# Kernel tuning notes

Measured on AMD Instinct MI355X. Metric: run time of the kernel, lower is better.

Reference implementation:

```python
import jax, jax.numpy as jnp
import numpy as np

TEMPERATURE = 0.07
BASE_TEMPERATURE = 0.07


def _supcon_one(feat, labels):
    # feat: [B, V, D], labels: [B]  (contrast_mode='all')
    B, V, D = feat.shape
    N = V * B
    # torch.cat(torch.unbind(feat, dim=1), dim=0): view-major ordering
    contrast = jnp.swapaxes(feat, 0, 1).reshape(N, D)  # [N, D]
    logits = jnp.einsum('nd,md->nm', contrast, contrast) / TEMPERATURE  # [N, N]
    # subtract detached row max for numerical stability
    logits = logits - jax.lax.stop_gradient(jnp.max(logits, axis=1, keepdims=True))
    pos = (labels[:, None] == labels[None, :]).astype(feat.dtype)  # [B, B]
    mask = jnp.tile(pos, (V, V))                                   # [N, N]
    logits_mask = 1.0 - jnp.eye(N, dtype=feat.dtype)               # zero out self-contrast
    mask = mask * logits_mask
    exp_logits = jnp.exp(logits) * logits_mask
    log_prob = logits - jnp.log(exp_logits.sum(axis=1, keepdims=True))
    mean_log_prob_pos = (mask * log_prob).sum(axis=1) / mask.sum(axis=1)
    return -(TEMPERATURE / BASE_TEMPERATURE) * mean_log_prob_pos.mean()


def setup_inputs() -> dict:
    key = jax.random.key(0)
    k1, k2 = jax.random.split(key)
    feat = jax.random.normal(k1, (16, 1024, 2, 128), dtype=jnp.float32)
    feat = feat / jnp.linalg.norm(feat, axis=-1, keepdims=True)  # unit-norm embeddings
    labels = jax.random.randint(k2, (16, 1024), 0, 64)
    return {"features": feat, "labels": labels}


def reference(features, labels):
    # vmap over the outer batch dim (replaces the Python loop), then mean
    losses = jax.vmap(_supcon_one)(features, labels)
    return losses.mean()
```

## Files before the change

### kernel.cpp

```cpp
#include <hip/hip_runtime.h>
#include <hip/hip_bf16.h>

#define TEMP_INV 14.285714285714286f
#define NBATCH 16
#define NROWS 2048
#define DDIM 128

typedef __attribute__((ext_vector_type(8))) short bf16x8;
typedef __attribute__((ext_vector_type(4))) float f32x4;

__global__ __launch_bounds__(256) void cast_reorder_kernel(
    const float* __restrict__ feat, __hip_bfloat16* __restrict__ out)
{
    int t = blockIdx.x * blockDim.x + threadIdx.x;
    int e = t << 2;
    int d = e & 127;
    int v = (e >> 7) & 1;
    int i = (e >> 8) & 1023;
    int b = e >> 18;
    const float4 f = *reinterpret_cast<const float4*>(feat + e);
    union { __hip_bfloat16 h[4]; uint2 u; } o;
    o.h[0] = __float2bfloat16(f.x);
    o.h[1] = __float2bfloat16(f.y);
    o.h[2] = __float2bfloat16(f.z);
    o.h[3] = __float2bfloat16(f.w);
    size_t oe = (size_t)(((b << 11) + (v << 10) + i)) * DDIM + d;
    *reinterpret_cast<uint2*>(out + oe) = o.u;
}

__global__ __launch_bounds__(256) void supcon_main_kernel(
    const __hip_bfloat16* __restrict__ contrast,
    const int* __restrict__ labels,
    float* __restrict__ out)
{
    __shared__ __hip_bfloat16 At[64 * DDIM];
    __shared__ __hip_bfloat16 Bt[128 * DDIM];
    __shared__ int slab[1024];
    __shared__ float rsum[64], rpos[64], rcnt[64];

    const int tid  = threadIdx.x;
    const int lane = tid & 63;
    const int w    = tid >> 6;
    const int wrow = w >> 1;
    const int wcol = w & 1;
    const int bx = blockIdx.x;
    const int b  = bx >> 5;
    const int rb = bx & 31;
    const int n0 = rb * 64;

    const __hip_bfloat16* cb = contrast + (size_t)b * NROWS * DDIM;
    const int* lb = labels + b * 1024;

    #pragma unroll
    for (int it = 0; it < 4; ++it) {
        int chunk = it * 256 + tid;
        int row = chunk >> 4, c = chunk & 15;
        uint4 vdat = *reinterpret_cast<const uint4*>(cb + (size_t)(n0 + row) * DDIM + c * 8);
        *reinterpret_cast<uint4*>(At + row * DDIM + ((c ^ (row & 7)) << 3)) = vdat;
    }
    #pragma unroll
    for (int it = 0; it < 4; ++it) slab[it * 256 + tid] = lb[it * 256 + tid];
    if (tid < 64) { rsum[tid] = 0.f; rpos[tid] = 0.f; rcnt[tid] = 0.f; }
    __syncthreads();

    bf16x8 afrag[2][4];
    #pragma unroll
    for (int fr = 0; fr < 2; ++fr) {
        int arow = wrow * 32 + fr * 16 + (lane & 15);
        #pragma unroll
        for (int ks = 0; ks < 4; ++ks) {
            int d = ks * 32 + ((lane >> 4) << 3);
            afrag[fr][ks] = *reinterpret_cast<const bf16x8*>(
                At + arow * DDIM + (d ^ ((arow & 7) << 3)));
        }
    }

    int rown[2][4], rowlab[2][4];
    #pragma unroll
    for (int fr = 0; fr < 2; ++fr)
        #pragma unroll
        for (int j = 0; j < 4; ++j) {
            int n = n0 + wrow * 32 + fr * 16 + ((lane >> 4) << 2) + j;
            rown[fr][j] = n;
            rowlab[fr][j] = slab[n & 1023];
        }

    float se[2][4] = {{0.f,0.f,0.f,0.f},{0.f,0.f,0.f,0.f}};
    float ps[2][4] = {{0.f,0.f,0.f,0.f},{0.f,0.f,0.f,0.f}};
    float pc[2][4] = {{0.f,0.f,0.f,0.f},{0.f,0.f,0.f,0.f}};

    for (int t = 0; t < 16; ++t) {
        const int m0 = t * 128;
        __syncthreads();
        #pragma unroll
        for (int it = 0; it < 8; ++it) {
            int chunk = it * 256 + tid;
            int row = chunk >> 4, c = chunk & 15;
            uint4 vdat = *reinterpret_cast<const uint4*>(cb + (size_t)(m0 + row) * DDIM + c * 8);
            *reinterpret_cast<uint4*>(Bt + row * DDIM + ((c ^ (row & 7)) << 3)) = vdat;
        }
        __syncthreads();

        f32x4 acc[2][4];
        #pragma unroll
        for (int fr = 0; fr < 2; ++fr)
            #pragma unroll
            for (int fc = 0; fc < 4; ++fc)
                acc[fr][fc] = (f32x4){0.f, 0.f, 0.f, 0.f};

        #pragma unroll
        for (int ks = 0; ks < 4; ++ks) {
            bf16x8 bfrag[4];
            #pragma unroll
            for (int fc = 0; fc < 4; ++fc) {
                int brow = wcol * 64 + fc * 16 + (lane & 15);
                int d = ks * 32 + ((lane >> 4) << 3);
                bfrag[fc] = *reinterpret_cast<const bf16x8*>(
                    Bt + brow * DDIM + (d ^ ((brow & 7) << 3)));
            }
            #pragma unroll
            for (int fr = 0; fr < 2; ++fr)
                #pragma unroll
                for (int fc = 0; fc < 4; ++fc)
                    acc[fr][fc] = __builtin_amdgcn_mfma_f32_16x16x32_bf16(
                        afrag[fr][ks], bfrag[fc], acc[fr][fc], 0, 0, 0);
        }

        #pragma unroll
        for (int fc = 0; fc < 4; ++fc) {
            int m = m0 + wcol * 64 + fc * 16 + (lane & 15);
            int lm = slab[m & 1023];
            #pragma unroll
            for (int fr = 0; fr < 2; ++fr) {
                #pragma unroll
                for (int j = 0; j < 4; ++j) {
                    float val = acc[fr][fc][j];
                    int n = rown[fr][j];
                    bool diag = (m == n);
                    float e = __expf(val * TEMP_INV - TEMP_INV);
                    if (diag) e = 0.f;
                    se[fr][j] += e;
                    bool p = (lm == rowlab[fr][j]) && !diag;
                    ps[fr][j] += p ? val : 0.f;
                    pc[fr][j] += p ? 1.f : 0.f;
                }
            }
        }
    }

    #pragma unroll
    for (int fr = 0; fr < 2; ++fr)
        #pragma unroll
        for (int j = 0; j < 4; ++j) {
            float s = se[fr][j], P = ps[fr][j], c = pc[fr][j];
            #pragma unroll
            for (int o = 1; o < 16; o <<= 1) {
                s += __shfl_xor(s, o);
                P += __shfl_xor(P, o);
                c += __shfl_xor(c, o);
            }
            if ((lane & 15) == 0) {
                int r = wrow * 32 + fr * 16 + ((lane >> 4) << 2) + j;
                atomicAdd(&rsum[r], s);
                atomicAdd(&rpos[r], P);
                atomicAdd(&rcnt[r], c);
            }
        }
    __syncthreads();

    if (tid < 64) {
        float row_loss = rpos[tid] * TEMP_INV / rcnt[tid] - TEMP_INV - __logf(rsum[tid]);
        float contrib = -row_loss * (1.0f / (float)(NBATCH * NROWS));
        #pragma unroll
        for (int o = 1; o < 64; o <<= 1) contrib += __shfl_xor(contrib, o);
        if (tid == 0) atomicAdd(out, contrib);
    }
}

extern "C" void kernel_launch(void* const* d_in, const int* in_sizes, int n_in,
                              void* d_out, int out_size, void* d_ws, size_t ws_size,
                              hipStream_t stream) {
    const float* feat  = (const float*)d_in[0];
    const int* labels  = (const int*)d_in[1];
    float* out = (float*)d_out;
    __hip_bfloat16* contrast = (__hip_bfloat16*)d_ws;

    hipMemsetAsync(d_out, 0, sizeof(float), stream);
    cast_reorder_kernel<<<4096, 256, 0, stream>>>(feat, contrast);
    supcon_main_kernel<<<512, 256, 0, stream>>>(contrast, labels, out);
}
```

Measured before the change: 108.2 us.

## Double-buffer B tiles via global_load_lds and move masking to finalize kernel

The main kernel now double-buffers the 128-row B tile in LDS, loading it with direct global-to-LDS loads so the next tile's fetch overlaps the current tile's MFMA work, and reuses the second buffer for the A tile. The inner epilogue drops the diagonal and positive-count logic: it always accumulates exp and the masked positive sum, records the diagonal value once per row, and uses exp2 with a fused multiply-add. Positive counts are derived from label histograms in a new finalize kernel, which also subtracts the diagonal contributions. Blocks are remapped by XCD so each batch's tiles share an L2. This adds a third kernel launch and workspace buffers, and precision may differ slightly from subtracting the diagonal term after the fact.

```diff
diff --git a/kernel.cpp b/kernel.cpp
--- a/kernel.cpp
+++ b/kernel.cpp
@@ -2,12 +2,18 @@
 #include <hip/hip_bf16.h>
 
 #define TEMP_INV 14.285714285714286f
+#define KL2E     20.60992947626f
+#define NC2      (-20.60992947626f)
 #define NBATCH 16
 #define NROWS 2048
 #define DDIM 128
 
 typedef __attribute__((ext_vector_type(8))) short bf16x8;
 typedef __attribute__((ext_vector_type(4))) float f32x4;
+
+#define GLOAD16(g, l) \
+  __builtin_amdgcn_global_load_lds((const __attribute__((address_space(1))) void*)(g), \
+                                   (__attribute__((address_space(3))) void*)(l), 16, 0, 0)
 
 __global__ __launch_bounds__(256) void cast_reorder_kernel(
     const float* __restrict__ feat, __hip_bfloat16* __restrict__ out)
@@ -31,75 +37,100 @@
 __global__ __launch_bounds__(256) void supcon_main_kernel(
     const __hip_bfloat16* __restrict__ contrast,
     const int* __restrict__ labels,
-    float* __restrict__ out)
+    float* __restrict__ rsum_ws, float* __restrict__ ps_ws, float* __restrict__ sd_ws)
 {
-    __shared__ __hip_bfloat16 At[64 * DDIM];
-    __shared__ __hip_bfloat16 Bt[128 * DDIM];
+    __shared__ __hip_bfloat16 Bt[2][128 * DDIM];
     __shared__ int slab[1024];
-    __shared__ float rsum[64], rpos[64], rcnt[64];
+    __shared__ float red_se[2][64], red_ps[2][64], red_sd[2][64];
 
     const int tid  = threadIdx.x;
     const int lane = tid & 63;
     const int w    = tid >> 6;
-    const int wrow = w >> 1;
-    const int wcol = w & 1;
-    const int bx = blockIdx.x;
-    const int b  = bx >> 5;
-    const int rb = bx & 31;
-    const int n0 = rb * 64;
+    const int wrow = w >> 1, wcol = w & 1;
+
+    const int bid = blockIdx.x;
+    const int xcd = bid & 7, idx = bid >> 3;
+    const int b   = xcd * 2 + (idx >> 5);
+    const int rb  = idx & 31;
+    const int n0  = rb * 64;
 
     const __hip_bfloat16* cb = contrast + (size_t)b * NROWS * DDIM;
     const int* lb = labels + b * 1024;
 
     #pragma unroll
-    for (int it = 0; it < 4; ++it) {
-        int chunk = it * 256 + tid;
-        int row = chunk >> 4, c = chunk & 15;
-        uint4 vdat = *reinterpret_cast<const uint4*>(cb + (size_t)(n0 + row) * DDIM + c * 8);
-        *reinterpret_cast<uint4*>(At + row * DDIM + ((c ^ (row & 7)) << 3)) = vdat;
-    }
-    #pragma unroll
     for (int it = 0; it < 4; ++it) slab[it * 256 + tid] = lb[it * 256 + tid];
-    if (tid < 64) { rsum[tid] = 0.f; rpos[tid] = 0.f; rcnt[tid] = 0.f; }
+
+    #pragma unroll
+    for (int c = 0; c < 4; ++c) {
+        const int r = (c * 4 + w) * 4 + (lane >> 4);
+        const int p = lane & 15;
+        GLOAD16(cb + (size_t)(n0 + r) * DDIM + ((p ^ (r & 7)) << 3),
+                (char*)(&Bt[1][0]) + (c * 4 + w) * 1024);
+    }
+    #pragma unroll
+    for (int c = 0; c < 8; ++c) {
+        const int r = (c * 4 + w) * 4 + (lane >> 4);
+        const int p = lane & 15;
+        GLOAD16(cb + (size_t)r * DDIM + ((p ^ (r & 7)) << 3),
+                (char*)(&Bt[0][0]) + (c * 4 + w) * 1024);
+    }
     __syncthreads();
 
     bf16x8 afrag[2][4];
     #pragma unroll
     for (int fr = 0; fr < 2; ++fr) {
-        int arow = wrow * 32 + fr * 16 + (lane & 15);
+        const int arow = wrow * 32 + fr * 16 + (lane & 15);
         #pragma unroll
         for (int ks = 0; ks < 4; ++ks) {
-            int d = ks * 32 + ((lane >> 4) << 3);
+            const int q = ks * 4 + (lane >> 4);
             afrag[fr][ks] = *reinterpret_cast<const bf16x8*>(
-                At + arow * DDIM + (d ^ ((arow & 7) << 3)));
-        }
-    }
-
+                (const char*)(&Bt[1][0]) + arow * 256 + ((q ^ (arow & 7)) << 4));
+        }
+    }
     int rown[2][4], rowlab[2][4];
     #pragma unroll
     for (int fr = 0; fr < 2; ++fr)
         #pragma unroll
         for (int j = 0; j < 4; ++j) {
-            int n = n0 + wrow * 32 + fr * 16 + ((lane >> 4) << 2) + j;
+            const int n = n0 + wrow * 32 + fr * 16 + ((lane >> 4) << 2) + j;
             rown[fr][j] = n;
             rowlab[fr][j] = slab[n & 1023];
         }
-
-    float se[2][4] = {{0.f,0.f,0.f,0.f},{0.f,0.f,0.f,0.f}};
-    float ps[2][4] = {{0.f,0.f,0.f,0.f},{0.f,0.f,0.f,0.f}};
-    float pc[2][4] = {{0.f,0.f,0.f,0.f},{0.f,0.f,0.f,0.f}};
+    __syncthreads();
+
+    const __hip_bfloat16* gsrc[8];
+    #pragma unroll
+    for (int c = 0; c < 8; ++c) {
+        const int r = (c * 4 + w) * 4 + (lane >> 4);
+        const int p = lane & 15;
+        gsrc[c] = cb + (size_t)(128 + r) * DDIM + ((p ^ (r & 7)) << 3);
+    }
+    int boff[4][4];
+    #pragma unroll
+    for (int fc = 0; fc < 4; ++fc) {
+        const int brow = wcol * 64 + fc * 16 + (lane & 15);
+        #pragma unroll
+        for (int ks = 0; ks < 4; ++ks) {
+            const int q = ks * 4 + (lane >> 4);
+            boff[fc][ks] = brow * 256 + ((q ^ (brow & 7)) << 4);
+        }
+    }
+
+    float se[2][4] = {{0,0,0,0},{0,0,0,0}};
+    float ps[2][4] = {{0,0,0,0},{0,0,0,0}};
+    float sd[2][4] = {{0,0,0,0},{0,0,0,0}};
+    const int tdiag = rb >> 1;
 
     for (int t = 0; t < 16; ++t) {
-        const int m0 = t * 128;
-        __syncthreads();
-        #pragma unroll
-        for (int it = 0; it < 8; ++it) {
-            int chunk = it * 256 + tid;
-            int row = chunk >> 4, c = chunk & 15;
-            uint4 vdat = *reinterpret_cast<const uint4*>(cb + (size_t)(m0 + row) * DDIM + c * 8);
-            *reinterpret_cast<uint4*>(Bt + row * DDIM + ((c ^ (row & 7)) << 3)) = vdat;
-        }
-        __syncthreads();
+        const int cur = t & 1;
+        if (t < 15) {
+            #pragma unroll
+            for (int c = 0; c < 8; ++c) {
+                GLOAD16(gsrc[c], (char*)(&Bt[cur ^ 1][0]) + (c * 4 + w) * 1024);
+                gsrc[c] += 128 * DDIM;
+            }
+        }
+        const char* base = (const char*)(&Bt[cur][0]);
 
         f32x4 acc[2][4];
         #pragma unroll
@@ -112,12 +143,8 @@
         for (int ks = 0; ks < 4; ++ks) {
             bf16x8 bfrag[4];
             #pragma unroll
-            for (int fc = 0; fc < 4; ++fc) {
-                int brow = wcol * 64 + fc * 16 + (lane & 15);
-                int d = ks * 32 + ((lane >> 4) << 3);
-                bfrag[fc] = *reinterpret_cast<const bf16x8*>(
-                    Bt + brow * DDIM + (d ^ ((brow & 7) << 3)));
-            }
+            for (int fc = 0; fc < 4; ++fc)
+                bfrag[fc] = *reinterpret_cast<const bf16x8*>(base + boff[fc][ks]);
             #pragma unroll
             for (int fr = 0; fr < 2; ++fr)
                 #pragma unroll
@@ -126,66 +153,107 @@
                         afrag[fr][ks], bfrag[fc], acc[fr][fc], 0, 0, 0);
         }
 
+        const int m0 = t * 128;
         #pragma unroll
         for (int fc = 0; fc < 4; ++fc) {
-            int m = m0 + wcol * 64 + fc * 16 + (lane & 15);
-            int lm = slab[m & 1023];
-            #pragma unroll
-            for (int fr = 0; fr < 2; ++fr) {
+            const int m = m0 + wcol * 64 + fc * 16 + (lane & 15);
+            const int lm = slab[m & 1023];
+            #pragma unroll
+            for (int fr = 0; fr < 2; ++fr)
                 #pragma unroll
                 for (int j = 0; j < 4; ++j) {
-                    float val = acc[fr][fc][j];
-                    int n = rown[fr][j];
-                    bool diag = (m == n);
-                    float e = __expf(val * TEMP_INV - TEMP_INV);
-                    if (diag) e = 0.f;
-                    se[fr][j] += e;
-                    bool p = (lm == rowlab[fr][j]) && !diag;
-                    ps[fr][j] += p ? val : 0.f;
-                    pc[fr][j] += p ? 1.f : 0.f;
+                    const float val = acc[fr][fc][j];
+                    se[fr][j] += exp2f(fmaf(val, KL2E, NC2));
+                    ps[fr][j] += (lm == rowlab[fr][j]) ? val : 0.f;
                 }
-            }
-        }
+        }
+        if (t == tdiag) {
+            #pragma unroll
+            for (int fc = 0; fc < 4; ++fc) {
+                const int m = m0 + wcol * 64 + fc * 16 + (lane & 15);
+                #pragma unroll
+                for (int fr = 0; fr < 2; ++fr)
+                    #pragma unroll
+                    for (int j = 0; j < 4; ++j)
+                        if (m == rown[fr][j]) sd[fr][j] = acc[fr][fc][j];
+            }
+        }
+        __syncthreads();
     }
 
     #pragma unroll
     for (int fr = 0; fr < 2; ++fr)
         #pragma unroll
         for (int j = 0; j < 4; ++j) {
-            float s = se[fr][j], P = ps[fr][j], c = pc[fr][j];
+            float s = se[fr][j], P = ps[fr][j], D = sd[fr][j];
             #pragma unroll
             for (int o = 1; o < 16; o <<= 1) {
                 s += __shfl_xor(s, o);
                 P += __shfl_xor(P, o);
-                c += __shfl_xor(c, o);
+                D += __shfl_xor(D, o);
             }
             if ((lane & 15) == 0) {
-                int r = wrow * 32 + fr * 16 + ((lane >> 4) << 2) + j;
-                atomicAdd(&rsum[r], s);
-                atomicAdd(&rpos[r], P);
-                atomicAdd(&rcnt[r], c);
-            }
-        }
-    __syncthreads();
-
+                const int r = wrow * 32 + fr * 16 + ((lane >> 4) << 2) + j;
+                red_se[wcol][r] = s; red_ps[wcol][r] = P; red_sd[wcol][r] = D;
+            }
+        }
+    __syncthreads();
     if (tid < 64) {
-        float row_loss = rpos[tid] * TEMP_INV / rcnt[tid] - TEMP_INV - __logf(rsum[tid]);
-        float contrib = -row_loss * (1.0f / (float)(NBATCH * NROWS));
-        #pragma unroll
-        for (int o = 1; o < 64; o <<= 1) contrib += __shfl_xor(contrib, o);
-        if (tid == 0) atomicAdd(out, contrib);
-    }
+        const int gn = b * NROWS + n0 + tid;
+        rsum_ws[gn] = red_se[0][tid] + red_se[1][tid];
+        ps_ws[gn]   = red_ps[0][tid] + red_ps[1][tid];
+        sd_ws[gn]   = red_sd[0][tid] + red_sd[1][tid];
+    }
+}
+
+__global__ __launch_bounds__(256) void finalize_kernel(
+    const int* __restrict__ labels,
+    const float* __restrict__ rsum_ws, const float* __restrict__ ps_ws,
+    const float* __restrict__ sd_ws, float* __restrict__ out)
+{
+    __shared__ int cnt_s[64];
+    __shared__ float wred[4];
+    const int tid = threadIdx.x, lane = tid & 63, wv = tid >> 6;
+    const int gid = blockIdx.x * 256 + tid;
+    const int b = gid >> 11, n = gid & 2047;
+    const int* lb = labels + b * 1024;
+
+    if (tid < 64) cnt_s[tid] = 0;
+    __syncthreads();
+    #pragma unroll
+    for (int k = 0; k < 4; ++k) atomicAdd(&cnt_s[lb[tid * 4 + k]], 1);
+    __syncthreads();
+
+    const int l = lb[n & 1023];
+    const float poscnt = (float)(2 * cnt_s[l] - 1);
+    const float D  = sd_ws[gid];
+    const float P  = ps_ws[gid] - D;
+    const float rs = rsum_ws[gid] - exp2f(fmaf(D, KL2E, NC2));
+    float mlpp = P * TEMP_INV / poscnt - TEMP_INV - __logf(rs);
+
+    #pragma unroll
+    for (int o = 1; o < 64; o <<= 1) mlpp += __shfl_xor(mlpp, o);
+    if (lane == 0) wred[wv] = mlpp;
+    __syncthreads();
+    if (tid == 0)
+        atomicAdd(out, -(wred[0] + wred[1] + wred[2] + wred[3]) * (1.0f / 32768.0f));
 }
 
 extern "C" void kernel_launch(void* const* d_in, const int* in_sizes, int n_in,
                               void* d_out, int out_size, void* d_ws, size_t ws_size,
                               hipStream_t stream) {
-    const float* feat  = (const float*)d_in[0];
-    const int* labels  = (const int*)d_in[1];
+    const float* feat = (const float*)d_in[0];
+    const int* labels = (const int*)d_in[1];
     float* out = (float*)d_out;
-    __hip_bfloat16* contrast = (__hip_bfloat16*)d_ws;
+
+    char* ws = (char*)d_ws;
+    __hip_bfloat16* contrast = (__hip_bfloat16*)ws;
+    float* rsum_ws = (float*)(ws + 8388608);
+    float* ps_ws   = (float*)(ws + 8519680);
+    float* sd_ws   = (float*)(ws + 8650752);
 
     hipMemsetAsync(d_out, 0, sizeof(float), stream);
     cast_reorder_kernel<<<4096, 256, 0, stream>>>(feat, contrast);
-    supcon_main_kernel<<<512, 256, 0, stream>>>(contrast, labels, out);
-}
+    supcon_main_kernel<<<512, 256, 0, stream>>>(contrast, labels, rsum_ws, ps_ws, sd_ws);
+    finalize_kernel<<<128, 256, 0, stream>>>(labels, rsum_ws, ps_ws, sd_ws, out);
+}
```

After: 112.1 us. +3.6%, slower.
